# Optimization experiments

Hardware: AMD Instinct MI355X
Metric: run time of the kernel (lower is better)

## Reference

```python
import jax, jax.numpy as jnp
import numpy as np

NEG_SLOPE = 0.2  # PyG GATConv default leaky_relu slope


def _add_self_loops(edge_index, num_nodes):
    loop = jnp.arange(num_nodes, dtype=edge_index.dtype)
    return jnp.concatenate([edge_index, jnp.stack([loop, loop])], axis=1)


def _gat_conv(x, edge_index, W, a_src, a_dst, b, heads, out_c):
    # x: [N, Fin]; W: [Fin, heads*out_c]; a_src/a_dst: [heads, out_c]; b: [heads*out_c]
    N = x.shape[0]
    h = (x @ W).reshape(N, heads, out_c)                       # [N,H,C]
    src, dst = edge_index[0], edge_index[1]
    alpha_src = jnp.einsum('nhc,hc->nh', h, a_src)             # [N,H]
    alpha_dst = jnp.einsum('nhc,hc->nh', h, a_dst)             # [N,H]
    e = jax.nn.leaky_relu(alpha_src[src] + alpha_dst[dst], NEG_SLOPE)  # [E,H]
    # segment softmax over edges grouped by destination node
    m = jax.ops.segment_max(e, dst, num_segments=N)
    m = jnp.where(jnp.isfinite(m), m, jnp.zeros_like(m))
    ex = jnp.exp(e - m[dst])
    denom = jax.ops.segment_sum(ex, dst, num_segments=N)
    alpha = ex / (denom[dst] + 1e-16)                          # [E,H]
    out = jax.ops.segment_sum(h[src] * alpha[:, :, None], dst, num_segments=N)
    return out.reshape(N, heads * out_c) + b


def setup_inputs() -> dict:
    key = jax.random.key(0)
    ks = jax.random.split(key, 16)
    N, E, FIN, HID, HEADS, OUT = 50000, 800000, 128, 32, 4, 64
    x = jax.random.normal(ks[0], (N, FIN), dtype=jnp.float32)
    edge_index = jax.random.randint(ks[1], (2, E), 0, N, dtype=jnp.int64)
    s = 0.1
    inp = {
        'x': x, 'edge_index': edge_index,
        'W0': jax.random.normal(ks[2], (FIN, HEADS * HID), jnp.float32) * s,
        'asrc0': jax.random.normal(ks[3], (HEADS, HID), jnp.float32) * s,
        'adst0': jax.random.normal(ks[4], (HEADS, HID), jnp.float32) * s,
        'b0': jnp.zeros((HEADS * HID,), jnp.float32),
        'W1': jax.random.normal(ks[5], (HEADS * HID, HEADS * HID), jnp.float32) * s,
        'asrc1': jax.random.normal(ks[6], (HEADS, HID), jnp.float32) * s,
        'adst1': jax.random.normal(ks[7], (HEADS, HID), jnp.float32) * s,
        'b1': jnp.zeros((HEADS * HID,), jnp.float32),
        'W2': jax.random.normal(ks[8], (HEADS * HID, OUT), jnp.float32) * s,
        'asrc2': jax.random.normal(ks[9], (1, OUT), jnp.float32) * s,
        'adst2': jax.random.normal(ks[10], (1, OUT), jnp.float32) * s,
        'b2': jnp.zeros((OUT,), jnp.float32),
    }
    return inp


def reference(x, edge_index, W0, asrc0, adst0, b0, W1, asrc1, adst1, b1, W2, asrc2, adst2, b2):
    # Dropout is identity in eval mode.
    N = x.shape[0]
    ei = _add_self_loops(edge_index, N)
    h = _gat_conv(x, ei, W0, asrc0, adst0, b0, heads=4, out_c=32)
    h = jax.nn.relu(h)
    h = _gat_conv(h, ei, W1, asrc1, adst1, b1, heads=4, out_c=32)
    h = jax.nn.relu(h)
    out = _gat_conv(h, ei, W2, asrc2, adst2, b2, heads=1, out_c=64)
    return out
```

## Files before the change

kernel.cpp:

```cpp
#include <hip/hip_runtime.h>


#define NEG_SLOPE 0.2f

typedef _Float16 f16;
typedef f16 f16x8 __attribute__((ext_vector_type(8)));
typedef f16 f16x4 __attribute__((ext_vector_type(4)));
typedef f16 f16x2 __attribute__((ext_vector_type(2)));
typedef float f32x4 __attribute__((ext_vector_type(4)));

__device__ __forceinline__ float lrelu(float v) { return v > 0.f ? v : NEG_SLOPE * v; }


__global__ void fill_zero_kernel(int* __restrict__ p, int n) {
    int i = blockIdx.x * blockDim.x + threadIdx.x;
    if (i < n) p[i] = 0;
}

__global__ __launch_bounds__(256) void bucket_count_kernel(const int* __restrict__ dst, int E,
                                                           int* __restrict__ bcount) {
    __shared__ int lh[256];
    lh[threadIdx.x] = 0;
    __syncthreads();
    int stride = gridDim.x * 256 * 4;
    for (int i = (blockIdx.x * 256 + threadIdx.x) * 4; i < E; i += stride) {
        int4 d = *(const int4*)&dst[i];
        atomicAdd(&lh[d.x >> 8], 1);
        atomicAdd(&lh[d.y >> 8], 1);
        atomicAdd(&lh[d.z >> 8], 1);
        atomicAdd(&lh[d.w >> 8], 1);
    }
    __syncthreads();
    int v = lh[threadIdx.x];
    if (v > 0) atomicAdd(&bcount[threadIdx.x], v);
}

__global__ __launch_bounds__(256) void bucket_scan_kernel(const int* __restrict__ bcount, int NBK,
                                                          int* __restrict__ bbase,
                                                          int* __restrict__ bcursor,
                                                          int* __restrict__ offsets, int N) {
    int t = threadIdx.x;
    int own = (t < NBK) ? bcount[t] : 0;
    int v = own;
    int lane = t & 63, wid = t >> 6;
#pragma unroll
    for (int off = 1; off < 64; off <<= 1) {
        int u = __shfl_up(v, off);
        if (lane >= off) v += u;
    }
    __shared__ int ws[4];
    if (lane == 63) ws[wid] = v;
    __syncthreads();
    int add = 0;
    for (int w = 0; w < wid; ++w) add += ws[w];
    v += add;
    int exc = v - own;
    if (t < NBK) {
        bbase[t] = exc;
        bcursor[t] = exc;
    }
    if (t == 255) {
        bbase[NBK] = v;
        offsets[N] = v;
    }
}

#define SC_TILE 4096
__global__ __launch_bounds__(256) void bucket_scatter_kernel(const int* __restrict__ src,
                                                             const int* __restrict__ dst, int E,
                                                             int* __restrict__ bcursor,
                                                             unsigned int* __restrict__ staging) {
    __shared__ int lh[256];
    __shared__ int lcur[256];
    int tid = threadIdx.x;
    lh[tid] = 0;
    __syncthreads();
    int base = blockIdx.x * SC_TILE + tid * 16;
    int sv[16], dv[16];
    bool act = base < E;
    if (act) {
#pragma unroll
        for (int q = 0; q < 4; ++q) {
            *(int4*)&sv[q * 4] = *(const int4*)&src[base + q * 4];
            *(int4*)&dv[q * 4] = *(const int4*)&dst[base + q * 4];
        }
#pragma unroll
        for (int j = 0; j < 16; ++j) atomicAdd(&lh[dv[j] >> 8], 1);
    }
    __syncthreads();
    int c = lh[tid];
    if (c > 0) lcur[tid] = atomicAdd(&bcursor[tid], c);
    __syncthreads();
    if (act) {
#pragma unroll
        for (int j = 0; j < 16; ++j) {
            int b = dv[j] >> 8;
            int pos = atomicAdd(&lcur[b], 1);
            staging[pos] = (unsigned int)sv[j] | ((unsigned int)(dv[j] & 255) << 16);
        }
    }
}

__global__ __launch_bounds__(256) void bucket_sort_kernel(const unsigned int* __restrict__ staging,
                                                          const int* __restrict__ bbase,
                                                          int* __restrict__ offsets,
                                                          int* __restrict__ ssrc, int N) {
    __shared__ int lh[256];
    __shared__ int ws[4];
    int b = blockIdx.x;
    int tid = threadIdx.x;
    int s = bbase[b], e = bbase[b + 1];
    int cnt = e - s;
    lh[tid] = 0;
    __syncthreads();
    for (int i = tid; i < cnt; i += 256) atomicAdd(&lh[staging[s + i] >> 16], 1);
    __syncthreads();
    int own = lh[tid];
    int v = own;
    int lane = tid & 63, wid = tid >> 6;
#pragma unroll
    for (int off = 1; off < 64; off <<= 1) {
        int u = __shfl_up(v, off);
        if (lane >= off) v += u;
    }
    if (lane == 63) ws[wid] = v;
    __syncthreads();
    int add = 0;
    for (int w = 0; w < wid; ++w) add += ws[w];
    int exc = v + add - own;
    int dstn = (b << 8) + tid;
    if (dstn < N) offsets[dstn] = s + exc;
    __syncthreads();
    lh[tid] = exc;
    __syncthreads();
    for (int i = tid; i < cnt; i += 256) {
        unsigned int rec = staging[s + i];
        int dlow = rec >> 16;
        int r = atomicAdd(&lh[dlow], 1);
        unsigned int full = (rec & 0xFFFFu) | ((unsigned int)((b << 8) | dlow) << 16);
        ssrc[s + r] = (int)full;
    }
}


__global__ void split_x_kernel(const float* __restrict__ x, f16* __restrict__ xh,
                               f16* __restrict__ xl, int total4) {
    int i = blockIdx.x * blockDim.x + threadIdx.x;
    if (i >= total4) return;
    float4 v = *(const float4*)&x[(size_t)i * 4];
    float vv[4] = {v.x, v.y, v.z, v.w};
    f16x4 h, l;
#pragma unroll
    for (int j = 0; j < 4; ++j) {
        f16 hj = (f16)vv[j];
        h[j] = hj;
        l[j] = (f16)(vv[j] - (float)hj);
    }
    *(f16x4*)&xh[(size_t)i * 4] = h;
    *(f16x4*)&xl[(size_t)i * 4] = l;
}

__global__ void split_w_kernel(const float* __restrict__ W0, const float* __restrict__ W1,
                               const float* __restrict__ W2, f16* __restrict__ w0h,
                               f16* __restrict__ w0l, f16* __restrict__ w1h,
                               f16* __restrict__ w1l, f16* __restrict__ w2h,
                               f16* __restrict__ w2l) {
    int idx = blockIdx.x * 256 + threadIdx.x;
    if (idx < 16384) {
        int k = idx >> 7, c = idx & 127;
        float v = W0[k * 128 + c];
        f16 h = (f16)v;
        w0h[c * 128 + k] = h;
        w0l[c * 128 + k] = (f16)(v - (float)h);
    } else if (idx < 32768) {
        int t = idx - 16384;
        int k = t >> 7, c = t & 127;
        float v = W1[k * 128 + c];
        f16 h = (f16)v;
        w1h[c * 128 + k] = h;
        w1l[c * 128 + k] = (f16)(v - (float)h);
    } else if (idx < 40960) {
        int t = idx - 32768;
        int k = t >> 6, c = t & 63;
        float v = W2[k * 64 + c];
        f16 h = (f16)v;
        w2h[c * 128 + k] = h;
        w2l[c * 128 + k] = (f16)(v - (float)h);
    }
}

template <int FOUT>
__global__ __launch_bounds__(256) void gemm_mfma_kernel(
    const f16* __restrict__ Ah, const f16* __restrict__ Al, const f16* __restrict__ Bh,
    const f16* __restrict__ Bl, f16* __restrict__ H16, int N) {
    constexpr int CT = FOUT / 16;
    __shared__ f16 lw[2][FOUT][72];
    int tid = threadIdx.x;
    int w = tid >> 6, lane = tid & 63;
    int quad = lane >> 4, m = lane & 15;
    int row0 = blockIdx.x * 64 + w * 16;
    int arow = row0 + m;
    if (arow >= N) arow = N - 1;
    const f16* aph = &Ah[(size_t)arow * 128 + quad * 8];
    const f16* apl = &Al[(size_t)arow * 128 + quad * 8];

    f32x4 acc[CT];
#pragma unroll
    for (int t = 0; t < CT; ++t) acc[t] = (f32x4){0.f, 0.f, 0.f, 0.f};

    for (int kh = 0; kh < 2; ++kh) {
        __syncthreads();
        for (int f = tid; f < FOUT * 8; f += 256) {
            int col = f >> 3, ch = f & 7;
            *(f16x8*)&lw[0][col][ch * 8] = *(const f16x8*)&Bh[(size_t)col * 128 + kh * 64 + ch * 8];
            *(f16x8*)&lw[1][col][ch * 8] = *(const f16x8*)&Bl[(size_t)col * 128 + kh * 64 + ch * 8];
        }
        __syncthreads();
#pragma unroll
        for (int kc = 0; kc < 2; ++kc) {
            f16x8 fah = *(const f16x8*)&aph[kh * 64 + kc * 32];
            f16x8 fal = *(const f16x8*)&apl[kh * 64 + kc * 32];
#pragma unroll
            for (int t = 0; t < CT; ++t) {
                f16x8 fbh = *(const f16x8*)&lw[0][t * 16 + m][kc * 32 + quad * 8];
                f16x8 fbl = *(const f16x8*)&lw[1][t * 16 + m][kc * 32 + quad * 8];
                acc[t] = __builtin_amdgcn_mfma_f32_16x16x32_f16(fah, fbh, acc[t], 0, 0, 0);
                acc[t] = __builtin_amdgcn_mfma_f32_16x16x32_f16(fal, fbh, acc[t], 0, 0, 0);
                acc[t] = __builtin_amdgcn_mfma_f32_16x16x32_f16(fah, fbl, acc[t], 0, 0, 0);
            }
        }
    }
#pragma unroll
    for (int r = 0; r < 4; ++r) {
        int row = row0 + quad * 4 + r;
        if (row < N) {
#pragma unroll
            for (int t = 0; t < CT; ++t)
                H16[(size_t)row * FOUT + t * 16 + m] = (f16)acc[t][r];
        }
    }
}

template <int H_, int C>
__global__ void alpha_kernel(const f16* __restrict__ h16, const float* __restrict__ a_src,
                             const float* __restrict__ a_dst, float* __restrict__ asrc,
                             float* __restrict__ adst, int N) {
    int idx = blockIdx.x * blockDim.x + threadIdx.x;
    if (idx >= N * H_) return;
    int n = idx / H_, h = idx % H_;
    const f16* hp = &h16[(size_t)n * H_ * C + h * C];
    const float* as = &a_src[h * C];
    const float* ad = &a_dst[h * C];
    float s1 = 0.f, s2 = 0.f;
#pragma unroll
    for (int c8 = 0; c8 < C / 8; ++c8) {
        f16x8 v = *(const f16x8*)&hp[c8 * 8];
#pragma unroll
        for (int j = 0; j < 8; ++j) {
            float vv = (float)v[j];
            s1 += vv * as[c8 * 8 + j];
            s2 += vv * ad[c8 * 8 + j];
        }
    }
    asrc[idx] = s1;
    adst[idx] = s2;
}

template <int H_>
__global__ void edgew_kernel(const int* __restrict__ ssrc, const float* __restrict__ asrc,
                             const float* __restrict__ adst, float* __restrict__ w, int E) {
    int k = blockIdx.x * 256 + threadIdx.x;
    if (k >= E) return;
    unsigned int rec = (unsigned int)ssrc[k];
    int s = rec & 0xFFFFu, d = rec >> 16;
    if (H_ == 4) {
        float4 a_s = *(const float4*)&asrc[s * 4];
        float4 a_dd = *(const float4*)&adst[d * 4];
        float4 a_sd = *(const float4*)&asrc[d * 4];
        w[0 * E + k] = __expf(lrelu(a_s.x + a_dd.x) - lrelu(a_sd.x + a_dd.x));
        w[1 * E + k] = __expf(lrelu(a_s.y + a_dd.y) - lrelu(a_sd.y + a_dd.y));
        w[2 * E + k] = __expf(lrelu(a_s.z + a_dd.z) - lrelu(a_sd.z + a_dd.z));
        w[3 * E + k] = __expf(lrelu(a_s.w + a_dd.w) - lrelu(a_sd.w + a_dd.w));
    } else {
        w[k] = __expf(lrelu(asrc[s] + adst[d]) - lrelu(asrc[d] + adst[d]));
    }
}

template <int H_, int C, bool RELU, bool SPLIT_OUT>
__global__ __launch_bounds__(256) void aggr_kernel(
    const f16* __restrict__ h16, const float* __restrict__ wedge,
    const float* __restrict__ bias, const int* __restrict__ offsets,
    const int* __restrict__ ssrc, float* __restrict__ outf, f16* __restrict__ outh,
    f16* __restrict__ outl, int N, int E) {
    constexpr int FOUT = H_ * C;
    constexpr int PER = FOUT / 64;
    int wid = threadIdx.x >> 6;
    int lane = threadIdx.x & 63;
    int n = blockIdx.x * 4 + wid;
    if (n >= N) return;
    int c0 = lane * PER;
    int head = c0 / C;
    const float* wb = wedge + head * E;

    float D = 1.f;
    float S0, S1 = 0.f;
    if (PER == 2) {
        f16x2 hv = *(const f16x2*)&h16[n * FOUT + c0];
        S0 = (float)hv[0];
        S1 = (float)hv[1];
    } else {
        S0 = (float)h16[n * FOUT + c0];
    }

    int k = offsets[n];
    const int e1 = offsets[n + 1];

    for (; k < e1 && (k & 3); ++k) {
        int s = ssrc[k] & 0xFFFF;
        float w = wb[k];
        D += w;
        if (PER == 2) {
            f16x2 hv = *(const f16x2*)&h16[s * FOUT + c0];
            S0 += w * (float)hv[0];
            S1 += w * (float)hv[1];
        } else {
            S0 += w * (float)h16[s * FOUT + c0];
        }
    }
    for (; k + 4 <= e1; k += 4) {
        int4 pk = *(const int4*)&ssrc[k];
        float4 wv = *(const float4*)&wb[k];
        int s0 = pk.x & 0xFFFF, s1 = pk.y & 0xFFFF, s2 = pk.z & 0xFFFF, s3 = pk.w & 0xFFFF;
        if (PER == 2) {
            f16x2 h0 = *(const f16x2*)&h16[s0 * FOUT + c0];
            f16x2 h1 = *(const f16x2*)&h16[s1 * FOUT + c0];
            f16x2 h2 = *(const f16x2*)&h16[s2 * FOUT + c0];
            f16x2 h3 = *(const f16x2*)&h16[s3 * FOUT + c0];
            D += (wv.x + wv.y) + (wv.z + wv.w);
            S0 += wv.x * (float)h0[0] + wv.y * (float)h1[0] + wv.z * (float)h2[0] +
                  wv.w * (float)h3[0];
            S1 += wv.x * (float)h0[1] + wv.y * (float)h1[1] + wv.z * (float)h2[1] +
                  wv.w * (float)h3[1];
        } else {
            float g0 = (float)h16[s0 * FOUT + c0];
            float g1 = (float)h16[s1 * FOUT + c0];
            float g2 = (float)h16[s2 * FOUT + c0];
            float g3 = (float)h16[s3 * FOUT + c0];
            D += (wv.x + wv.y) + (wv.z + wv.w);
            S0 += wv.x * g0 + wv.y * g1 + wv.z * g2 + wv.w * g3;
        }
    }
    for (; k < e1; ++k) {
        int s = ssrc[k] & 0xFFFF;
        float w = wb[k];
        D += w;
        if (PER == 2) {
            f16x2 hv = *(const f16x2*)&h16[s * FOUT + c0];
            S0 += w * (float)hv[0];
            S1 += w * (float)hv[1];
        } else {
            S0 += w * (float)h16[s * FOUT + c0];
        }
    }

    float inv = 1.f / (D + 1e-16f);
    float v0 = S0 * inv + bias[c0];
    if (RELU) v0 = fmaxf(v0, 0.f);
    if (SPLIT_OUT) {
        float v1 = S1 * inv + bias[c0 + 1];
        if (RELU) v1 = fmaxf(v1, 0.f);
        f16 h0 = (f16)v0, h1 = (f16)v1;
        f16x2 hh = {h0, h1};
        f16x2 ll = {(f16)(v0 - (float)h0), (f16)(v1 - (float)h1)};
        *(f16x2*)&outh[n * FOUT + c0] = hh;
        *(f16x2*)&outl[n * FOUT + c0] = ll;
    } else if (PER == 2) {
        float v1 = S1 * inv + bias[c0 + 1];
        if (RELU) v1 = fmaxf(v1, 0.f);
        *(float2*)&outf[n * FOUT + c0] = make_float2(v0, v1);
    } else {
        outf[n * FOUT + c0] = v0;
    }
}

extern "C" void kernel_launch(void* const* d_in, const int* in_sizes, int n_in,
                              void* d_out, int out_size, void* d_ws, size_t ws_size,
                              hipStream_t stream) {
    const float* x = (const float*)d_in[0];
    const int* ei = (const int*)d_in[1];
    const float* W0 = (const float*)d_in[2];
    const float* as0 = (const float*)d_in[3];
    const float* ad0 = (const float*)d_in[4];
    const float* b0 = (const float*)d_in[5];
    const float* W1 = (const float*)d_in[6];
    const float* as1 = (const float*)d_in[7];
    const float* ad1 = (const float*)d_in[8];
    const float* b1 = (const float*)d_in[9];
    const float* W2 = (const float*)d_in[10];
    const float* as2 = (const float*)d_in[11];
    const float* ad2 = (const float*)d_in[12];
    const float* b2 = (const float*)d_in[13];

    const int N = in_sizes[0] / 128;
    const int E = in_sizes[1] / 2;
    const int NBK = (N + 255) >> 8;

    float* aS = (float*)d_ws;
    float* aD = aS + (size_t)N * 4;
    f16* h16 = (f16*)(aD + (size_t)N * 4);
    f16* xh = h16 + (size_t)N * 128;
    f16* xl = xh + (size_t)N * 128;
    f16* w0h = xl + (size_t)N * 128;
    f16* w0l = w0h + 16384;
    f16* w1h = w0l + 16384;
    f16* w1l = w1h + 16384;
    f16* w2h = w1l + 16384;
    f16* w2l = w2h + 8192;
    int* offsets = (int*)(w2l + 8192);
    int* ssrc = offsets + N + 1;
    unsigned int* staging = (unsigned int*)(ssrc + E);
    float* wedge = (float*)(staging + E);
    int* bcount = (int*)(wedge + (size_t)E * 4);
    int* bbase = bcount + NBK;
    int* bcursor = bbase + NBK + 1;

    fill_zero_kernel<<<1, 256, 0, stream>>>(bcount, NBK);
    bucket_count_kernel<<<196, 256, 0, stream>>>(ei + E, E, bcount);
    bucket_scan_kernel<<<1, 256, 0, stream>>>(bcount, NBK, bbase, bcursor, offsets, N);
    bucket_scatter_kernel<<<(E + SC_TILE - 1) / SC_TILE, 256, 0, stream>>>(ei, ei + E, E, bcursor,
                                                                           staging);
    bucket_sort_kernel<<<NBK, 256, 0, stream>>>(staging, bbase, offsets, ssrc, N);

    split_x_kernel<<<(N * 32 + 255) / 256, 256, 0, stream>>>(x, xh, xl, N * 32);
    split_w_kernel<<<160, 256, 0, stream>>>(W0, W1, W2, w0h, w0l, w1h, w1l, w2h, w2l);

    const int gGemm = (N + 63) / 64;
    const int gAggr = (N + 3) / 4;
    const int gE = (E + 255) / 256;

    gemm_mfma_kernel<128><<<gGemm, 256, 0, stream>>>(xh, xl, w0h, w0l, h16, N);
    alpha_kernel<4, 32><<<(N * 4 + 255) / 256, 256, 0, stream>>>(h16, as0, ad0, aS, aD, N);
    edgew_kernel<4><<<gE, 256, 0, stream>>>(ssrc, aS, aD, wedge, E);
    aggr_kernel<4, 32, true, true><<<gAggr, 256, 0, stream>>>(h16, wedge, b0, offsets, ssrc,
                                                              nullptr, xh, xl, N, E);
    gemm_mfma_kernel<128><<<gGemm, 256, 0, stream>>>(xh, xl, w1h, w1l, h16, N);
    alpha_kernel<4, 32><<<(N * 4 + 255) / 256, 256, 0, stream>>>(h16, as1, ad1, aS, aD, N);
    edgew_kernel<4><<<gE, 256, 0, stream>>>(ssrc, aS, aD, wedge, E);
    aggr_kernel<4, 32, true, true><<<gAggr, 256, 0, stream>>>(h16, wedge, b1, offsets, ssrc,
                                                              nullptr, xh, xl, N, E);
    gemm_mfma_kernel<64><<<gGemm, 256, 0, stream>>>(xh, xl, w2h, w2l, h16, N);
    alpha_kernel<1, 64><<<(N + 255) / 256, 256, 0, stream>>>(h16, as2, ad2, aS, aD, N);
    edgew_kernel<1><<<gE, 256, 0, stream>>>(ssrc, aS, aD, wedge, E);
    aggr_kernel<1, 64, false, false><<<gAggr, 256, 0, stream>>>(h16, wedge, b2, offsets, ssrc,
                                                                (float*)d_out, nullptr, nullptr,
                                                                N, E);
}
```

Measured before the change: 348.7 us.

## Gather 16-byte feature rows per lane and interleave edge weights per head

The aggregation kernel now gives each lane 8 contiguous fp16 features (16-byte loads). The wavefront is split into edge groups that each walk a strided subset of a node's incoming edges, and partial sums are combined with xor shuffles at the end. Edge weights are stored interleaved as [E,4] instead of head-major, so the edge-weight kernel writes one float4 per edge. The aim is fewer, wider gather transactions and more edges in flight per wave, at the cost of a cross-lane reduction and more registers.

```diff
diff --git a/kernel.cpp b/kernel.cpp
--- a/kernel.cpp
+++ b/kernel.cpp
@@ -277,10 +277,12 @@
         float4 a_s = *(const float4*)&asrc[s * 4];
         float4 a_dd = *(const float4*)&adst[d * 4];
         float4 a_sd = *(const float4*)&asrc[d * 4];
-        w[0 * E + k] = __expf(lrelu(a_s.x + a_dd.x) - lrelu(a_sd.x + a_dd.x));
-        w[1 * E + k] = __expf(lrelu(a_s.y + a_dd.y) - lrelu(a_sd.y + a_dd.y));
-        w[2 * E + k] = __expf(lrelu(a_s.z + a_dd.z) - lrelu(a_sd.z + a_dd.z));
-        w[3 * E + k] = __expf(lrelu(a_s.w + a_dd.w) - lrelu(a_sd.w + a_dd.w));
+        float4 o;
+        o.x = __expf(lrelu(a_s.x + a_dd.x) - lrelu(a_sd.x + a_dd.x));
+        o.y = __expf(lrelu(a_s.y + a_dd.y) - lrelu(a_sd.y + a_dd.y));
+        o.z = __expf(lrelu(a_s.z + a_dd.z) - lrelu(a_sd.z + a_dd.z));
+        o.w = __expf(lrelu(a_s.w + a_dd.w) - lrelu(a_sd.w + a_dd.w));
+        *(float4*)&w[(size_t)k * 4] = o;
     } else {
         w[k] = __expf(lrelu(asrc[s] + adst[d]) - lrelu(asrc[d] + adst[d]));
     }
@@ -291,95 +293,89 @@
     const f16* __restrict__ h16, const float* __restrict__ wedge,
     const float* __restrict__ bias, const int* __restrict__ offsets,
     const int* __restrict__ ssrc, float* __restrict__ outf, f16* __restrict__ outh,
-    f16* __restrict__ outl, int N, int E) {
+    f16* __restrict__ outl, int N) {
     constexpr int FOUT = H_ * C;
-    constexpr int PER = FOUT / 64;
+    constexpr int LPG = FOUT / 8;
+    constexpr int GROUPS = 64 / LPG;
+    constexpr int UN = (GROUPS == 4) ? 4 : 2;
     int wid = threadIdx.x >> 6;
     int lane = threadIdx.x & 63;
     int n = blockIdx.x * 4 + wid;
     if (n >= N) return;
-    int c0 = lane * PER;
+    int g = lane / LPG;
+    int t = lane % LPG;
+    int c0 = t * 8;
     int head = c0 / C;
-    const float* wb = wedge + head * E;
-
-    float D = 1.f;
-    float S0, S1 = 0.f;
-    if (PER == 2) {
-        f16x2 hv = *(const f16x2*)&h16[n * FOUT + c0];
-        S0 = (float)hv[0];
-        S1 = (float)hv[1];
-    } else {
-        S0 = (float)h16[n * FOUT + c0];
-    }
-
-    int k = offsets[n];
-    const int e1 = offsets[n + 1];
-
-    for (; k < e1 && (k & 3); ++k) {
+
+    float D = 0.f;
+    float S[8];
+#pragma unroll
+    for (int j = 0; j < 8; ++j) S[j] = 0.f;
+    if (g == 0) {
+        D = 1.f;
+        f16x8 hv = *(const f16x8*)&h16[n * FOUT + c0];
+#pragma unroll
+        for (int j = 0; j < 8; ++j) S[j] = (float)hv[j];
+    }
+
+    int e1 = offsets[n + 1];
+    int k = offsets[n] + g;
+
+    for (; k + (UN - 1) * GROUPS < e1; k += UN * GROUPS) {
+        float wv[UN];
+        f16x8 hvv[UN];
+#pragma unroll
+        for (int u = 0; u < UN; ++u) {
+            int kk = k + u * GROUPS;
+            int s = ssrc[kk] & 0xFFFF;
+            wv[u] = (H_ == 4) ? wedge[(size_t)kk * 4 + head] : wedge[kk];
+            hvv[u] = *(const f16x8*)&h16[s * FOUT + c0];
+        }
+#pragma unroll
+        for (int u = 0; u < UN; ++u) {
+            D += wv[u];
+#pragma unroll
+            for (int j = 0; j < 8; ++j) S[j] += wv[u] * (float)hvv[u][j];
+        }
+    }
+    for (; k < e1; k += GROUPS) {
         int s = ssrc[k] & 0xFFFF;
-        float w = wb[k];
+        float w = (H_ == 4) ? wedge[(size_t)k * 4 + head] : wedge[k];
+        f16x8 hv = *(const f16x8*)&h16[s * FOUT + c0];
         D += w;
-        if (PER == 2) {
-            f16x2 hv = *(const f16x2*)&h16[s * FOUT + c0];
-            S0 += w * (float)hv[0];
-            S1 += w * (float)hv[1];
+#pragma unroll
+        for (int j = 0; j < 8; ++j) S[j] += w * (float)hv[j];
+    }
+
+#pragma unroll
+    for (int mask = LPG; mask < 64; mask <<= 1) {
+        D += __shfl_xor(D, mask);
+#pragma unroll
+        for (int j = 0; j < 8; ++j) S[j] += __shfl_xor(S[j], mask);
+    }
+
+    if (g == 0) {
+        float inv = 1.f / (D + 1e-16f);
+        float v[8];
+#pragma unroll
+        for (int j = 0; j < 8; ++j) {
+            v[j] = S[j] * inv + bias[c0 + j];
+            if (RELU) v[j] = fmaxf(v[j], 0.f);
+        }
+        if (SPLIT_OUT) {
+            f16x8 hh, ll;
+#pragma unroll
+            for (int j = 0; j < 8; ++j) {
+                f16 h = (f16)v[j];
+                hh[j] = h;
+                ll[j] = (f16)(v[j] - (float)h);
+            }
+            *(f16x8*)&outh[n * FOUT + c0] = hh;
+            *(f16x8*)&outl[n * FOUT + c0] = ll;
         } else {
-            S0 += w * (float)h16[s * FOUT + c0];
-        }
-    }
-    for (; k + 4 <= e1; k += 4) {
-        int4 pk = *(const int4*)&ssrc[k];
-        float4 wv = *(const float4*)&wb[k];
-        int s0 = pk.x & 0xFFFF, s1 = pk.y & 0xFFFF, s2 = pk.z & 0xFFFF, s3 = pk.w & 0xFFFF;
-        if (PER == 2) {
-            f16x2 h0 = *(const f16x2*)&h16[s0 * FOUT + c0];
-            f16x2 h1 = *(const f16x2*)&h16[s1 * FOUT + c0];
-            f16x2 h2 = *(const f16x2*)&h16[s2 * FOUT + c0];
-            f16x2 h3 = *(const f16x2*)&h16[s3 * FOUT + c0];
-            D += (wv.x + wv.y) + (wv.z + wv.w);
-            S0 += wv.x * (float)h0[0] + wv.y * (float)h1[0] + wv.z * (float)h2[0] +
-                  wv.w * (float)h3[0];
-            S1 += wv.x * (float)h0[1] + wv.y * (float)h1[1] + wv.z * (float)h2[1] +
-                  wv.w * (float)h3[1];
-        } else {
-            float g0 = (float)h16[s0 * FOUT + c0];
-            float g1 = (float)h16[s1 * FOUT + c0];
-            float g2 = (float)h16[s2 * FOUT + c0];
-            float g3 = (float)h16[s3 * FOUT + c0];
-            D += (wv.x + wv.y) + (wv.z + wv.w);
-            S0 += wv.x * g0 + wv.y * g1 + wv.z * g2 + wv.w * g3;
-        }
-    }
-    for (; k < e1; ++k) {
-        int s = ssrc[k] & 0xFFFF;
-        float w = wb[k];
-        D += w;
-        if (PER == 2) {
-            f16x2 hv = *(const f16x2*)&h16[s * FOUT + c0];
-            S0 += w * (float)hv[0];
-            S1 += w * (float)hv[1];
-        } else {
-            S0 += w * (float)h16[s * FOUT + c0];
-        }
-    }
-
-    float inv = 1.f / (D + 1e-16f);
-    float v0 = S0 * inv + bias[c0];
-    if (RELU) v0 = fmaxf(v0, 0.f);
-    if (SPLIT_OUT) {
-        float v1 = S1 * inv + bias[c0 + 1];
-        if (RELU) v1 = fmaxf(v1, 0.f);
-        f16 h0 = (f16)v0, h1 = (f16)v1;
-        f16x2 hh = {h0, h1};
-        f16x2 ll = {(f16)(v0 - (float)h0), (f16)(v1 - (float)h1)};
-        *(f16x2*)&outh[n * FOUT + c0] = hh;
-        *(f16x2*)&outl[n * FOUT + c0] = ll;
-    } else if (PER == 2) {
-        float v1 = S1 * inv + bias[c0 + 1];
-        if (RELU) v1 = fmaxf(v1, 0.f);
-        *(float2*)&outf[n * FOUT + c0] = make_float2(v0, v1);
-    } else {
-        outf[n * FOUT + c0] = v0;
+            *(float4*)&outf[n * FOUT + c0] = make_float4(v[0], v[1], v[2], v[3]);
+            *(float4*)&outf[n * FOUT + c0 + 4] = make_float4(v[4], v[5], v[6], v[7]);
+        }
     }
 }
 
@@ -442,16 +438,16 @@
     alpha_kernel<4, 32><<<(N * 4 + 255) / 256, 256, 0, stream>>>(h16, as0, ad0, aS, aD, N);
     edgew_kernel<4><<<gE, 256, 0, stream>>>(ssrc, aS, aD, wedge, E);
     aggr_kernel<4, 32, true, true><<<gAggr, 256, 0, stream>>>(h16, wedge, b0, offsets, ssrc,
-                                                              nullptr, xh, xl, N, E);
+                                                              nullptr, xh, xl, N);
     gemm_mfma_kernel<128><<<gGemm, 256, 0, stream>>>(xh, xl, w1h, w1l, h16, N);
     alpha_kernel<4, 32><<<(N * 4 + 255) / 256, 256, 0, stream>>>(h16, as1, ad1, aS, aD, N);
     edgew_kernel<4><<<gE, 256, 0, stream>>>(ssrc, aS, aD, wedge, E);
     aggr_kernel<4, 32, true, true><<<gAggr, 256, 0, stream>>>(h16, wedge, b1, offsets, ssrc,
-                                                              nullptr, xh, xl, N, E);
+                                                              nullptr, xh, xl, N);
     gemm_mfma_kernel<64><<<gGemm, 256, 0, stream>>>(xh, xl, w2h, w2l, h16, N);
     alpha_kernel<1, 64><<<(N + 255) / 256, 256, 0, stream>>>(h16, as2, ad2, aS, aD, N);
     edgew_kernel<1><<<gE, 256, 0, stream>>>(ssrc, aS, aD, wedge, E);
     aggr_kernel<1, 64, false, false><<<gAggr, 256, 0, stream>>>(h16, wedge, b2, offsets, ssrc,
                                                                 (float*)d_out, nullptr, nullptr,
-                                                                N, E);
-}
+                                                                N);
+}
```

Result: faster. 321.0 us (-7.9%).
